# Performance work log

Measured on AMD Instinct MI355X. Metric: run time of the kernel, lower is better.

## Reference

```python
import jax, jax.numpy as jnp
from jax import lax
import numpy as np

B, T, IN, H = 512, 512, 32, 64


def _lstm_layer(x_seq, W_ih, W_hh, b_ih, b_hh):
    """One PyTorch-convention LSTM layer. x_seq: [B, T, in] -> hs: [B, T, H].
    Gate order i, f, g, o; zero initial (h, c)."""
    Bb = x_seq.shape[0]
    Hh = W_hh.shape[1]
    # Precompute input-to-gate projections for the whole sequence (one big GEMM).
    xg = jnp.einsum('bti,gi->btg', x_seq, W_ih) + b_ih + b_hh  # [B, T, 4H]

    def step(carry, xg_t):
        h, c = carry
        gates = xg_t + h @ W_hh.T  # [B, 4H]
        i, f, g, o = jnp.split(gates, 4, axis=-1)
        i = jax.nn.sigmoid(i)
        f = jax.nn.sigmoid(f)
        g = jnp.tanh(g)
        o = jax.nn.sigmoid(o)
        c = f * c + i * g
        h = o * jnp.tanh(c)
        return (h, c), h

    h0 = jnp.zeros((Bb, Hh), x_seq.dtype)
    (_, _), hs = lax.scan(step, (h0, h0), jnp.swapaxes(xg, 0, 1))  # hs: [T, B, H]
    return jnp.swapaxes(hs, 0, 1)


def setup_inputs() -> dict:
    key = jax.random.key(0)
    ks = jax.random.split(key, 11)
    s_in = 1.0 / np.sqrt(H)
    return {
        'x': jax.random.normal(ks[0], (B, T, IN), jnp.float32),
        'W_ih0': jax.random.normal(ks[1], (4 * H, IN), jnp.float32) * s_in,
        'W_hh0': jax.random.normal(ks[2], (4 * H, H), jnp.float32) * s_in,
        'b_ih0': jax.random.normal(ks[3], (4 * H,), jnp.float32) * s_in,
        'b_hh0': jax.random.normal(ks[4], (4 * H,), jnp.float32) * s_in,
        'W_ih1': jax.random.normal(ks[5], (4 * H, H), jnp.float32) * s_in,
        'W_hh1': jax.random.normal(ks[6], (4 * H, H), jnp.float32) * s_in,
        'b_ih1': jax.random.normal(ks[7], (4 * H,), jnp.float32) * s_in,
        'b_hh1': jax.random.normal(ks[8], (4 * H,), jnp.float32) * s_in,
        'W_fc': jax.random.normal(ks[9], (1, H), jnp.float32) * s_in,
        'b_fc': jax.random.normal(ks[10], (1,), jnp.float32) * s_in,
    }


def reference(x, W_ih0, W_hh0, b_ih0, b_hh0, W_ih1, W_hh1, b_ih1, b_hh1, W_fc, b_fc):
    h1 = _lstm_layer(x, W_ih0, W_hh0, b_ih0, b_hh0)   # [B, T, H]
    # inter-layer dropout and final dropout are identity in eval mode
    h2 = _lstm_layer(h1, W_ih1, W_hh1, b_ih1, b_hh1)  # [B, T, H]
    last = h2[:, -1, :]                               # [B, H]
    return last @ W_fc.T + b_fc                       # [B, 1]
```

## Files before the change

### kernel.cpp

```cpp
#include <hip/hip_runtime.h>

#define T_STEPS 512
#define BATCH   512
#define INPUT   32
#define HID     64
#define NGATES  256
#define CH      64

__device__ __forceinline__ float fast_sigmoid(float x) {
    return 1.0f / (1.0f + __expf(-x));
}
__device__ __forceinline__ float fast_tanh(float x) {
    return 1.0f - 2.0f / (1.0f + __expf(2.0f * x));
}

__global__ __launch_bounds__(256, 2)
void lstm_layer0(const float* __restrict__ x,
                 const float* __restrict__ W_ih,
                 const float* __restrict__ W_hh,
                 const float* __restrict__ b_ih,
                 const float* __restrict__ b_hh,
                 float* __restrict__ h1out)
{
    __shared__ float xs[T_STEPS * INPUT];
    __shared__ float gates_s[NGATES];
    __shared__ float hbuf[HID];

    const int b = blockIdx.x;
    const int g = threadIdx.x;

    float wih[INPUT];
    float whh[HID];
    {
        const float4* wr = reinterpret_cast<const float4*>(W_ih + (size_t)g * INPUT);
        #pragma unroll
        for (int k = 0; k < INPUT / 4; ++k) {
            float4 v = wr[k];
            wih[4*k+0] = v.x; wih[4*k+1] = v.y; wih[4*k+2] = v.z; wih[4*k+3] = v.w;
        }
        const float4* hr = reinterpret_cast<const float4*>(W_hh + (size_t)g * HID);
        #pragma unroll
        for (int k = 0; k < HID / 4; ++k) {
            float4 v = hr[k];
            whh[4*k+0] = v.x; whh[4*k+1] = v.y; whh[4*k+2] = v.z; whh[4*k+3] = v.w;
        }
    }
    const float bias = b_ih[g] + b_hh[g];

    {
        const float4* src = reinterpret_cast<const float4*>(x + (size_t)b * T_STEPS * INPUT);
        float4* dst = reinterpret_cast<float4*>(xs);
        for (int i = threadIdx.x; i < T_STEPS * INPUT / 4; i += 256) dst[i] = src[i];
    }
    if (g < HID) hbuf[g] = 0.0f;
    float c = 0.0f;
    __syncthreads();

    for (int t = 0; t < T_STEPS; ++t) {
        float acc = bias;
        const float* xt = xs + t * INPUT;
        #pragma unroll
        for (int k = 0; k < INPUT; ++k) acc = fmaf(wih[k], xt[k], acc);
        #pragma unroll
        for (int k = 0; k < HID; ++k)   acc = fmaf(whh[k], hbuf[k], acc);

        float a = (g >= 2 * HID && g < 3 * HID) ? fast_tanh(acc) : fast_sigmoid(acc);
        gates_s[g] = a;
        __syncthreads();

        if (g < HID) {
            float i_ = gates_s[g];
            float f_ = gates_s[HID + g];
            float g_ = gates_s[2 * HID + g];
            float o_ = gates_s[3 * HID + g];
            c = fmaf(f_, c, i_ * g_);
            float h = o_ * fast_tanh(c);
            hbuf[g] = h;
            h1out[((size_t)b * T_STEPS + t) * HID + g] = h;
        }
        __syncthreads();
    }
}

__global__ __launch_bounds__(256, 2)
void lstm_layer1(const float* __restrict__ h1,
                 const float* __restrict__ W_ih,
                 const float* __restrict__ W_hh,
                 const float* __restrict__ b_ih,
                 const float* __restrict__ b_hh,
                 const float* __restrict__ W_fc,
                 const float* __restrict__ b_fc,
                 float* __restrict__ out)
{
    __shared__ float xs[CH * HID];
    __shared__ float gates_s[NGATES];
    __shared__ float hbuf[HID];

    const int b = blockIdx.x;
    const int g = threadIdx.x;

    float wih[HID];
    float whh[HID];
    {
        const float4* xr = reinterpret_cast<const float4*>(W_ih + (size_t)g * HID);
        #pragma unroll
        for (int k = 0; k < HID / 4; ++k) {
            float4 v = xr[k];
            wih[4*k+0] = v.x; wih[4*k+1] = v.y; wih[4*k+2] = v.z; wih[4*k+3] = v.w;
        }
        const float4* hr = reinterpret_cast<const float4*>(W_hh + (size_t)g * HID);
        #pragma unroll
        for (int k = 0; k < HID / 4; ++k) {
            float4 v = hr[k];
            whh[4*k+0] = v.x; whh[4*k+1] = v.y; whh[4*k+2] = v.z; whh[4*k+3] = v.w;
        }
    }
    const float bias = b_ih[g] + b_hh[g];

    if (g < HID) hbuf[g] = 0.0f;
    float c = 0.0f;
    __syncthreads();

    for (int t = 0; t < T_STEPS; ++t) {
        if ((t & (CH - 1)) == 0) {
            const float4* src = reinterpret_cast<const float4*>(
                h1 + ((size_t)b * T_STEPS + t) * HID);
            float4* dst = reinterpret_cast<float4*>(xs);
            for (int i = threadIdx.x; i < CH * HID / 4; i += 256) dst[i] = src[i];
            __syncthreads();
        }
        const float* xt = xs + (t & (CH - 1)) * HID;

        float acc = bias;
        #pragma unroll
        for (int k = 0; k < HID; ++k) acc = fmaf(wih[k], xt[k], acc);
        #pragma unroll
        for (int k = 0; k < HID; ++k) acc = fmaf(whh[k], hbuf[k], acc);

        float a = (g >= 2 * HID && g < 3 * HID) ? fast_tanh(acc) : fast_sigmoid(acc);
        gates_s[g] = a;
        __syncthreads();

        if (g < HID) {
            float i_ = gates_s[g];
            float f_ = gates_s[HID + g];
            float g_ = gates_s[2 * HID + g];
            float o_ = gates_s[3 * HID + g];
            c = fmaf(f_, c, i_ * g_);
            float h = o_ * fast_tanh(c);
            hbuf[g] = h;
        }
        __syncthreads();
    }

    if (g < HID) {
        float v = hbuf[g] * W_fc[g];
        #pragma unroll
        for (int off = 32; off > 0; off >>= 1) v += __shfl_down(v, off);
        if (g == 0) out[b] = v + b_fc[0];
    }
}

extern "C" void kernel_launch(void* const* d_in, const int* in_sizes, int n_in,
                              void* d_out, int out_size, void* d_ws, size_t ws_size,
                              hipStream_t stream) {
    const float* x     = (const float*)d_in[0];
    const float* W_ih0 = (const float*)d_in[1];
    const float* W_hh0 = (const float*)d_in[2];
    const float* b_ih0 = (const float*)d_in[3];
    const float* b_hh0 = (const float*)d_in[4];
    const float* W_ih1 = (const float*)d_in[5];
    const float* W_hh1 = (const float*)d_in[6];
    const float* b_ih1 = (const float*)d_in[7];
    const float* b_hh1 = (const float*)d_in[8];
    const float* W_fc  = (const float*)d_in[9];
    const float* b_fc  = (const float*)d_in[10];

    float* out = (float*)d_out;
    float* h1  = (float*)d_ws;

    lstm_layer0<<<BATCH, 256, 0, stream>>>(x, W_ih0, W_hh0, b_ih0, b_hh0, h1);
    lstm_layer1<<<BATCH, 256, 0, stream>>>(h1, W_ih1, W_hh1, b_ih1, b_hh1,
                                           W_fc, b_fc, out);
}
```

Baseline: 871.8 us.

## Precompute input projections per 64-step chunk, keep only W_hh in registers

```diff
diff --git a/kernel.cpp b/kernel.cpp
--- a/kernel.cpp
+++ b/kernel.cpp
@@ -2,10 +2,11 @@
 
 #define T_STEPS 512
 #define BATCH   512
-#define INPUT   32
 #define HID     64
 #define NGATES  256
 #define CH      64
+
+#define PIN(x) asm volatile("" : "+v"(x))
 
 __device__ __forceinline__ float fast_sigmoid(float x) {
     return 1.0f / (1.0f + __expf(-x));
@@ -14,105 +15,34 @@
     return 1.0f - 2.0f / (1.0f + __expf(2.0f * x));
 }
 
+template<int K_IN, bool LAST>
 __global__ __launch_bounds__(256, 2)
-void lstm_layer0(const float* __restrict__ x,
-                 const float* __restrict__ W_ih,
-                 const float* __restrict__ W_hh,
-                 const float* __restrict__ b_ih,
-                 const float* __restrict__ b_hh,
-                 float* __restrict__ h1out)
+void lstm_layer(const float* __restrict__ xin,
+                const float* __restrict__ W_ih,
+                const float* __restrict__ W_hh,
+                const float* __restrict__ b_ih,
+                const float* __restrict__ b_hh,
+                float* __restrict__ hout,
+                const float* __restrict__ W_fc,
+                const float* __restrict__ b_fc,
+                float* __restrict__ fcout)
 {
-    __shared__ float xs[T_STEPS * INPUT];
-    __shared__ float gates_s[NGATES];
-    __shared__ float hbuf[HID];
+    __shared__ __align__(16) float xg_s[CH * NGATES];
+    __shared__ __align__(16) float gates_s[NGATES];
+    __shared__ __align__(16) float hbuf[HID];
 
-    const int b = blockIdx.x;
-    const int g = threadIdx.x;
+    const int b    = blockIdx.x;
+    const int g    = threadIdx.x;
+    const int lane = g & 63;
 
-    float wih[INPUT];
-    float whh[HID];
+    float4 whh4[HID / 4];
     {
-        const float4* wr = reinterpret_cast<const float4*>(W_ih + (size_t)g * INPUT);
-        #pragma unroll
-        for (int k = 0; k < INPUT / 4; ++k) {
-            float4 v = wr[k];
-            wih[4*k+0] = v.x; wih[4*k+1] = v.y; wih[4*k+2] = v.z; wih[4*k+3] = v.w;
-        }
         const float4* hr = reinterpret_cast<const float4*>(W_hh + (size_t)g * HID);
         #pragma unroll
-        for (int k = 0; k < HID / 4; ++k) {
-            float4 v = hr[k];
-            whh[4*k+0] = v.x; whh[4*k+1] = v.y; whh[4*k+2] = v.z; whh[4*k+3] = v.w;
-        }
-    }
-    const float bias = b_ih[g] + b_hh[g];
-
-    {
-        const float4* src = reinterpret_cast<const float4*>(x + (size_t)b * T_STEPS * INPUT);
-        float4* dst = reinterpret_cast<float4*>(xs);
-        for (int i = threadIdx.x; i < T_STEPS * INPUT / 4; i += 256) dst[i] = src[i];
-    }
-    if (g < HID) hbuf[g] = 0.0f;
-    float c = 0.0f;
-    __syncthreads();
-
-    for (int t = 0; t < T_STEPS; ++t) {
-        float acc = bias;
-        const float* xt = xs + t * INPUT;
-        #pragma unroll
-        for (int k = 0; k < INPUT; ++k) acc = fmaf(wih[k], xt[k], acc);
-        #pragma unroll
-        for (int k = 0; k < HID; ++k)   acc = fmaf(whh[k], hbuf[k], acc);
-
-        float a = (g >= 2 * HID && g < 3 * HID) ? fast_tanh(acc) : fast_sigmoid(acc);
-        gates_s[g] = a;
-        __syncthreads();
-
-        if (g < HID) {
-            float i_ = gates_s[g];
-            float f_ = gates_s[HID + g];
-            float g_ = gates_s[2 * HID + g];
-            float o_ = gates_s[3 * HID + g];
-            c = fmaf(f_, c, i_ * g_);
-            float h = o_ * fast_tanh(c);
-            hbuf[g] = h;
-            h1out[((size_t)b * T_STEPS + t) * HID + g] = h;
-        }
-        __syncthreads();
-    }
-}
-
-__global__ __launch_bounds__(256, 2)
-void lstm_layer1(const float* __restrict__ h1,
-                 const float* __restrict__ W_ih,
-                 const float* __restrict__ W_hh,
-                 const float* __restrict__ b_ih,
-                 const float* __restrict__ b_hh,
-                 const float* __restrict__ W_fc,
-                 const float* __restrict__ b_fc,
-                 float* __restrict__ out)
-{
-    __shared__ float xs[CH * HID];
-    __shared__ float gates_s[NGATES];
-    __shared__ float hbuf[HID];
-
-    const int b = blockIdx.x;
-    const int g = threadIdx.x;
-
-    float wih[HID];
-    float whh[HID];
-    {
-        const float4* xr = reinterpret_cast<const float4*>(W_ih + (size_t)g * HID);
+        for (int k = 0; k < HID / 4; ++k) whh4[k] = hr[k];
         #pragma unroll
         for (int k = 0; k < HID / 4; ++k) {
-            float4 v = xr[k];
-            wih[4*k+0] = v.x; wih[4*k+1] = v.y; wih[4*k+2] = v.z; wih[4*k+3] = v.w;
-        }
-        const float4* hr = reinterpret_cast<const float4*>(W_hh + (size_t)g * HID);
-        #pragma unroll
-        for (int k = 0; k < HID / 4; ++k) {
-            float4 v = hr[k];
-            whh[4*k+0] = v.x; whh[4*k+1] = v.y; whh[4*k+2] = v.z; whh[4*k+3] = v.w;
+            PIN(whh4[k].x); PIN(whh4[k].y); PIN(whh4[k].z); PIN(whh4[k].w);
         }
     }
     const float bias = b_ih[g] + b_hh[g];
@@ -121,43 +51,67 @@
     float c = 0.0f;
     __syncthreads();
 
-    for (int t = 0; t < T_STEPS; ++t) {
-        if ((t & (CH - 1)) == 0) {
-            const float4* src = reinterpret_cast<const float4*>(
-                h1 + ((size_t)b * T_STEPS + t) * HID);
-            float4* dst = reinterpret_cast<float4*>(xs);
-            for (int i = threadIdx.x; i < CH * HID / 4; i += 256) dst[i] = src[i];
+    for (int c0 = 0; c0 < T_STEPS; c0 += CH) {
+        {
+            float4 wih4[K_IN / 4];
+            const float4* wr = reinterpret_cast<const float4*>(W_ih + (size_t)g * K_IN);
+            #pragma unroll
+            for (int k = 0; k < K_IN / 4; ++k) wih4[k] = wr[k];
+
+            const float* xrow = xin + ((size_t)b * T_STEPS + c0) * K_IN;
+            for (int tm = 0; tm < CH; ++tm) {
+                float a0 = bias, a1 = 0.0f, a2 = 0.0f, a3 = 0.0f;
+                const float* xp = xrow + tm * K_IN;
+                #pragma unroll
+                for (int k = 0; k < K_IN / 4; ++k) {
+                    a0 = fmaf(wih4[k].x, xp[4 * k + 0], a0);
+                    a1 = fmaf(wih4[k].y, xp[4 * k + 1], a1);
+                    a2 = fmaf(wih4[k].z, xp[4 * k + 2], a2);
+                    a3 = fmaf(wih4[k].w, xp[4 * k + 3], a3);
+                }
+                xg_s[tm * NGATES + g] = (a0 + a1) + (a2 + a3);
+            }
+        }
+        __syncthreads();
+
+        for (int tm = 0; tm < CH; ++tm) {
+            const float4* hb4 = reinterpret_cast<const float4*>(hbuf);
+            float a0 = xg_s[tm * NGATES + g], a1 = 0.0f, a2 = 0.0f, a3 = 0.0f;
+            #pragma unroll
+            for (int k = 0; k < HID / 4; ++k) {
+                float4 hv = hb4[k];
+                a0 = fmaf(whh4[k].x, hv.x, a0);
+                a1 = fmaf(whh4[k].y, hv.y, a1);
+                a2 = fmaf(whh4[k].z, hv.z, a2);
+                a3 = fmaf(whh4[k].w, hv.w, a3);
+            }
+            float acc = (a0 + a1) + (a2 + a3);
+
+            float a = ((g >> 6) == 2) ? fast_tanh(acc) : fast_sigmoid(acc);
+            gates_s[g] = a;
+            __syncthreads();
+
+            float i_ = gates_s[lane];
+            float f_ = gates_s[HID + lane];
+            float g_ = gates_s[2 * HID + lane];
+            float o_ = gates_s[3 * HID + lane];
+            c = fmaf(f_, c, i_ * g_);
+            float h = o_ * fast_tanh(c);
+            if (g < HID) {
+                hbuf[g] = h;
+                if (!LAST) hout[((size_t)b * T_STEPS + (c0 + tm)) * HID + g] = h;
+            }
             __syncthreads();
         }
-        const float* xt = xs + (t & (CH - 1)) * HID;
-
-        float acc = bias;
-        #pragma unroll
-        for (int k = 0; k < HID; ++k) acc = fmaf(wih[k], xt[k], acc);
-        #pragma unroll
-        for (int k = 0; k < HID; ++k) acc = fmaf(whh[k], hbuf[k], acc);
-
-        float a = (g >= 2 * HID && g < 3 * HID) ? fast_tanh(acc) : fast_sigmoid(acc);
-        gates_s[g] = a;
-        __syncthreads();
-
-        if (g < HID) {
-            float i_ = gates_s[g];
-            float f_ = gates_s[HID + g];
-            float g_ = gates_s[2 * HID + g];
-            float o_ = gates_s[3 * HID + g];
-            c = fmaf(f_, c, i_ * g_);
-            float h = o_ * fast_tanh(c);
-            hbuf[g] = h;
-        }
-        __syncthreads();
     }
 
-    if (g < HID) {
-        float v = hbuf[g] * W_fc[g];
-        #pragma unroll
-        for (int off = 32; off > 0; off >>= 1) v += __shfl_down(v, off);
-        if (g == 0) out[b] = v + b_fc[0];
+    if (LAST) {
+        if (g < HID) {
+            float v = hbuf[g] * W_fc[g];
+            #pragma unroll
+            for (int off = 32; off; off >>= 1) v += __shfl_down(v, off);
+            if (g == 0) fcout[b] = v + b_fc[0];
+        }
     }
 }
 
@@ -179,7 +133,8 @@
     float* out = (float*)d_out;
     float* h1  = (float*)d_ws;
 
-    lstm_layer0<<<BATCH, 256, 0, stream>>>(x, W_ih0, W_hh0, b_ih0, b_hh0, h1);
-    lstm_layer1<<<BATCH, 256, 0, stream>>>(h1, W_ih1, W_hh1, b_ih1, b_hh1,
-                                           W_fc, b_fc, out);
+    lstm_layer<32, false><<<BATCH, 256, 0, stream>>>(
+        x, W_ih0, W_hh0, b_ih0, b_hh0, h1, nullptr, nullptr, nullptr);
+    lstm_layer<64, true><<<BATCH, 256, 0, stream>>>(
+        h1, W_ih1, W_hh1, b_ih1, b_hh1, nullptr, W_fc, b_fc, out);
 }
```

Result: slower. 1.125 ms (+29.1%).
